# Kernel optimization log

Measured on AMD Instinct MI355X. Metric: run time of the kernel, lower is better.

The kernel has to match this reference:

```python
import jax, jax.numpy as jnp
import numpy as np

N = 100000
E = 1600000
D_IN = 128
HID = 128
LN_EPS = 1e-5
GIN_EPS = 0.0  # PyG GINConv default eps


def setup_inputs() -> dict:
    key = jax.random.key(0)
    ks = jax.random.split(key, 8)
    x = jax.random.normal(ks[0], (N, D_IN), dtype=jnp.float32)
    edge_index = jax.random.randint(ks[1], (2, E), 0, N, dtype=jnp.int64)
    s1 = 1.0 / np.sqrt(D_IN)
    s2 = 1.0 / np.sqrt(HID)
    W1 = jax.random.uniform(ks[2], (D_IN, HID), jnp.float32, -s1, s1)
    b1 = jnp.zeros((HID,), jnp.float32)
    W2 = jax.random.uniform(ks[3], (HID, HID), jnp.float32, -s2, s2)
    b2 = jnp.zeros((HID,), jnp.float32)
    gamma = jnp.ones((HID,), jnp.float32)
    beta = jnp.zeros((HID,), jnp.float32)
    Wres = jax.random.uniform(ks[4], (D_IN, HID), jnp.float32, -s1, s1)
    bres = jnp.zeros((HID,), jnp.float32)
    return {"x": x, "edge_index": edge_index, "W1": W1, "b1": b1,
            "W2": W2, "b2": b2, "gamma": gamma, "beta": beta,
            "Wres": Wres, "bres": bres}


def reference(x, edge_index, W1, b1, W2, b2, gamma, beta, Wres, bres):
    src, dst = edge_index[0], edge_index[1]
    # GIN sum aggregation: scatter-add source features onto targets. [N, D_IN]
    agg = jax.ops.segment_sum(x[src], dst, num_segments=N)
    h = (1.0 + GIN_EPS) * x + agg
    # GIN MLP: Linear -> ReLU -> Linear
    h = jax.nn.relu(h @ W1 + b1) @ W2 + b2
    # LayerNorm over hidden dim
    mu = jnp.mean(h, axis=-1, keepdims=True)
    var = jnp.mean(jnp.square(h - mu), axis=-1, keepdims=True)
    h = (h - mu) * jax.lax.rsqrt(var + LN_EPS) * gamma + beta
    # dropout p=0 is identity; residual linear path
    return h + (x @ Wres + bres)
```

## Files before the change

kernel.cpp:

```cpp
#include <hip/hip_runtime.h>

#define NN 100000
#define NE 1600000
#define D 128
#define RT 64
#define NB 196
#define CAP 9216
#define PADB 136
#define PB 12503
#define BUCKB 391

typedef unsigned short u16;
typedef __attribute__((ext_vector_type(8))) short bf16x8;
typedef __attribute__((ext_vector_type(4))) float f32x4;

__device__ __forceinline__ u16 f2bf(float f) {
  unsigned int u = __float_as_uint(f);
  u += 0x7fffu + ((u >> 16) & 1u);
  return (u16)(u >> 16);
}

__global__ __launch_bounds__(256) void prep_bucket_kernel(
    const float* __restrict__ x, const int* __restrict__ ei,
    const float* __restrict__ W1, const float* __restrict__ W2,
    const float* __restrict__ Wres,
    u16* __restrict__ xh, u16* __restrict__ wt,
    int* __restrict__ tail, unsigned* __restrict__ buf) {
  __shared__ int lhist[NB], lbase[NB];
  int b = blockIdx.x;
  int t = threadIdx.x;
  if (b < 12500) {
    int q = b * 256 + t;
    float4 v = ((const float4*)x)[q];
    uint2 pk;
    pk.x = (unsigned)f2bf(v.x) | ((unsigned)f2bf(v.y) << 16);
    pk.y = (unsigned)f2bf(v.z) | ((unsigned)f2bf(v.w) << 16);
    ((uint2*)xh)[q] = pk;
  } else if (b < PB) {
    const float* W = (b == 12500) ? Wres : (b == 12501) ? W1 : W2;
    u16* dst = wt + (size_t)(b - 12500) * 16384;
    for (int i = t; i < 16384; i += 256) {
      int n = i >> 7, k = i & 127;
      dst[i] = f2bf(W[k * 128 + n]);
    }
  } else {
    size_t e0 = (size_t)(b - PB) * 4096;
    int s[16], d[16];
    for (int j = t; j < NB; j += 256) lhist[j] = 0;
    __syncthreads();
#pragma unroll
    for (int k = 0; k < 16; ++k) {
      size_t e = e0 + t + (size_t)k * 256;
      if (e < NE) {
        d[k] = ei[NE + e];
        s[k] = ei[e];
        atomicAdd(&lhist[d[k] >> 9], 1);
      } else {
        d[k] = -1;
      }
    }
    __syncthreads();
    for (int j = t; j < NB; j += 256) {
      int c = lhist[j];
      lbase[j] = c ? atomicAdd(&tail[j], c) : 0;
      lhist[j] = 0;
    }
    __syncthreads();
#pragma unroll
    for (int k = 0; k < 16; ++k) {
      if (d[k] >= 0) {
        int bk = d[k] >> 9;
        int r = lbase[bk] + atomicAdd(&lhist[bk], 1);
        if (r < CAP)
          buf[(size_t)bk * CAP + r] = (unsigned)s[k] | ((unsigned)(d[k] & 511) << 17);
      }
    }
  }
}

__global__ __launch_bounds__(512) void build_csr(const unsigned* __restrict__ buf,
                                                 const int* __restrict__ tail,
                                                 int* __restrict__ cnt,
                                                 int* __restrict__ start,
                                                 int* __restrict__ csr) {
  __shared__ int lhist[512], lpre[512], lsum[64];
  int b = blockIdx.x, t = threadIdx.x;
  int nE = tail[b];
  if (nE > CAP) nE = CAP;
  size_t bBase = (size_t)b * CAP;
  lhist[t] = 0;
  __syncthreads();
  for (int i = t; i < nE; i += 512)
    atomicAdd(&lhist[buf[bBase + i] >> 17], 1);
  __syncthreads();
  if (t < 64) {
    int s = 0;
#pragma unroll
    for (int k = 0; k < 8; ++k) { int v = lhist[t * 8 + k]; lpre[t * 8 + k] = s; s += v; }
    lsum[t] = s;
  }
  __syncthreads();
  if (t == 0) {
    int s = 0;
    for (int k = 0; k < 64; ++k) { int v = lsum[k]; lsum[k] = s; s += v; }
  }
  __syncthreads();
  if (t < 64) {
    int o = lsum[t];
#pragma unroll
    for (int k = 0; k < 8; ++k) lpre[t * 8 + k] += o;
  }
  __syncthreads();
  int node = (b << 9) + t;
  if (node < NN) {
    cnt[node] = lhist[t];
    start[node] = (int)bBase + lpre[t];
  }
  lhist[t] = 0;
  __syncthreads();
  for (int i = t; i < nE; i += 512) {
    unsigned e = buf[bBase + i];
    int dl = e >> 17;
    int r = atomicAdd(&lhist[dl], 1);
    csr[bBase + lpre[dl] + r] = (int)(e & 0x1FFFFu);
  }
}

#define BFACC8(aL, aH, v)                                  \
  { aL.x += __uint_as_float((v).x << 16);                  \
    aL.y += __uint_as_float((v).x & 0xffff0000u);          \
    aL.z += __uint_as_float((v).y << 16);                  \
    aL.w += __uint_as_float((v).y & 0xffff0000u);          \
    aH.x += __uint_as_float((v).z << 16);                  \
    aH.y += __uint_as_float((v).z & 0xffff0000u);          \
    aH.z += __uint_as_float((v).w << 16);                  \
    aH.w += __uint_as_float((v).w & 0xffff0000u); }

__global__ __launch_bounds__(256, 6) void gather_kernel(const float* __restrict__ x,
                                                        const u16* __restrict__ xh,
                                                        const int* __restrict__ cnt,
                                                        const int* __restrict__ start,
                                                        const int* __restrict__ csr,
                                                        u16* __restrict__ h0h) {
  int g = blockIdx.x * 16 + (threadIdx.x >> 4);
  if (g >= NN) return;
  int lane = threadIdx.x & 15;
  int fo = lane * 8;
  int n = cnt[g];
  const int* sp = csr + start[g];

  float4 aL0 = make_float4(0.f, 0.f, 0.f, 0.f);
  float4 aH0 = aL0, aL1 = aL0, aH1 = aL0;

  int nfull = n & ~3;
  if (nfull > 0) {
    int s0 = sp[0], s1 = sp[1], s2 = sp[2], s3 = sp[3];
    uint4 v0 = *(const uint4*)&xh[(size_t)s0 * D + fo];
    uint4 v1 = *(const uint4*)&xh[(size_t)s1 * D + fo];
    uint4 v2 = *(const uint4*)&xh[(size_t)s2 * D + fo];
    uint4 v3 = *(const uint4*)&xh[(size_t)s3 * D + fo];
#pragma unroll 2
    for (int j = 4; j < nfull; j += 4) {
      int t0 = sp[j], t1 = sp[j + 1], t2 = sp[j + 2], t3 = sp[j + 3];
      uint4 w0 = *(const uint4*)&xh[(size_t)t0 * D + fo];
      uint4 w1 = *(const uint4*)&xh[(size_t)t1 * D + fo];
      uint4 w2 = *(const uint4*)&xh[(size_t)t2 * D + fo];
      uint4 w3 = *(const uint4*)&xh[(size_t)t3 * D + fo];
      BFACC8(aL0, aH0, v0); BFACC8(aL1, aH1, v1);
      BFACC8(aL0, aH0, v2); BFACC8(aL1, aH1, v3);
      v0 = w0; v1 = w1; v2 = w2; v3 = w3;
    }
    BFACC8(aL0, aH0, v0); BFACC8(aL1, aH1, v1);
    BFACC8(aL0, aH0, v2); BFACC8(aL1, aH1, v3);
  }
  for (int j = nfull; j < n; ++j) {
    uint4 v0 = *(const uint4*)&xh[(size_t)sp[j] * D + fo];
    BFACC8(aL0, aH0, v0);
  }

  const float* xp = &x[(size_t)g * D + fo];
  float4 x0 = *(const float4*)xp;
  float4 x1 = *(const float4*)(xp + 4);
  float h0 = x0.x + aL0.x + aL1.x;
  float h1 = x0.y + aL0.y + aL1.y;
  float h2 = x0.z + aL0.z + aL1.z;
  float h3 = x0.w + aL0.w + aL1.w;
  float h4 = x1.x + aH0.x + aH1.x;
  float h5 = x1.y + aH0.y + aH1.y;
  float h6 = x1.z + aH0.z + aH1.z;
  float h7 = x1.w + aH0.w + aH1.w;
  uint4 pk;
  pk.x = (unsigned)f2bf(h0) | ((unsigned)f2bf(h1) << 16);
  pk.y = (unsigned)f2bf(h2) | ((unsigned)f2bf(h3) << 16);
  pk.z = (unsigned)f2bf(h4) | ((unsigned)f2bf(h5) << 16);
  pk.w = (unsigned)f2bf(h6) | ((unsigned)f2bf(h7) << 16);
  *(uint4*)&h0h[(size_t)g * 256 + fo] = pk;
}

__global__ __launch_bounds__(256, 3) void fused_kernel(
    const u16* __restrict__ xh, const u16* __restrict__ h0h,
    const u16* __restrict__ wt,
    const float* __restrict__ b1, const float* __restrict__ b2,
    const float* __restrict__ gamma, const float* __restrict__ beta,
    const float* __restrict__ bres, float* __restrict__ out) {
  __shared__ u16 Ws[128 * PADB];
  __shared__ u16 Hs[RT * PADB];

  const int t = threadIdx.x;
  const int w = t >> 6;
  const int lane = t & 63;
  const int quad = lane >> 4;
  const int l16 = lane & 15;
  const int row0 = blockIdx.x * RT;

  auto stageW = [&](const u16* __restrict__ src) {
#pragma unroll
    for (int i = 0; i < 16; ++i) {
      int v = t + i * 256;
      int r = v >> 5;
      int c4 = (v & 31) << 2;
      *(uint2*)&Ws[r * PADB + c4] = *(const uint2*)&src[r * D + c4];
    }
  };

  f32x4 acc[8], accR[8];
  f32x4 zz = {0.f, 0.f, 0.f, 0.f};
#pragma unroll
  for (int i = 0; i < 8; ++i) { acc[i] = zz; accR[i] = zz; }

  auto gemmGA = [&](const u16* __restrict__ Ag, int astride, f32x4 (&dd)[8]) {
    bf16x8 af[4];
    int ar = row0 + w * 16 + l16;
    if (ar > NN - 1) ar = NN - 1;
#pragma unroll
    for (int s = 0; s < 4; ++s)
      af[s] = *(const bf16x8*)&Ag[(size_t)ar * astride + s * 32 + quad * 8];
#pragma unroll
    for (int nt = 0; nt < 8; ++nt) {
      const u16* wp = &Ws[(nt * 16 + l16) * PADB + quad * 8];
#pragma unroll
      for (int s = 0; s < 4; ++s) {
        bf16x8 bf = *(const bf16x8*)&wp[s * 32];
        dd[nt] = __builtin_amdgcn_mfma_f32_16x16x32_bf16(af[s], bf, dd[nt], 0, 0, 0);
      }
    }
  };
  auto gemmLA = [&](f32x4 (&dd)[8]) {
    bf16x8 af[4];
#pragma unroll
    for (int s = 0; s < 4; ++s)
      af[s] = *(const bf16x8*)&Hs[(w * 16 + l16) * PADB + s * 32 + quad * 8];
#pragma unroll
    for (int nt = 0; nt < 8; ++nt) {
      const u16* wp = &Ws[(nt * 16 + l16) * PADB + quad * 8];
#pragma unroll
      for (int s = 0; s < 4; ++s) {
        bf16x8 bf = *(const bf16x8*)&wp[s * 32];
        dd[nt] = __builtin_amdgcn_mfma_f32_16x16x32_bf16(af[s], bf, dd[nt], 0, 0, 0);
      }
    }
  };

  stageW(wt);
  __syncthreads();
  gemmGA(xh, D, accR);
  __syncthreads();
  stageW(wt + 16384);
  __syncthreads();
  gemmGA(h0h, 256, acc);
  __syncthreads();

#pragma unroll
  for (int nt = 0; nt < 8; ++nt) {
    int col = nt * 16 + l16;
    float bb = b1[col];
#pragma unroll
    for (int r = 0; r < 4; ++r) {
      float hv = acc[nt][r] + bb;
      hv = hv > 0.f ? hv : 0.f;
      Hs[(w * 16 + quad * 4 + r) * PADB + col] = f2bf(hv);
      acc[nt][r] = 0.f;
    }
  }
  stageW(wt + 32768);
  __syncthreads();
  gemmLA(acc);

  float b2v[8], gv[8], bev[8], brv[8];
#pragma unroll
  for (int nt = 0; nt < 8; ++nt) {
    int col = nt * 16 + l16;
    b2v[nt] = b2[col];
    gv[nt] = gamma[col];
    bev[nt] = beta[col];
    brv[nt] = bres[col];
  }
#pragma unroll
  for (int r = 0; r < 4; ++r) {
    float s = 0.f, s2 = 0.f;
#pragma unroll
    for (int nt = 0; nt < 8; ++nt) {
      float h = acc[nt][r] + b2v[nt];
      s += h;
      s2 += h * h;
    }
    for (int m = 1; m <= 8; m <<= 1) {
      s += __shfl_xor(s, m);
      s2 += __shfl_xor(s2, m);
    }
    float mu = s * 0.0078125f;
    float var = s2 * 0.0078125f - mu * mu;
    float rs = rsqrtf(var + 1e-5f);
    int row = row0 + w * 16 + quad * 4 + r;
    if (row < NN) {
#pragma unroll
      for (int nt = 0; nt < 8; ++nt) {
        float h = acc[nt][r] + b2v[nt];
        out[(size_t)row * D + nt * 16 + l16] =
            (h - mu) * rs * gv[nt] + bev[nt] + accR[nt][r] + brv[nt];
      }
    }
  }
}

extern "C" void kernel_launch(void* const* d_in, const int* in_sizes, int n_in,
                              void* d_out, int out_size, void* d_ws, size_t ws_size,
                              hipStream_t stream) {
  const float* x     = (const float*)d_in[0];
  const int*   ei    = (const int*)d_in[1];
  const float* W1    = (const float*)d_in[2];
  const float* b1    = (const float*)d_in[3];
  const float* W2    = (const float*)d_in[4];
  const float* b2    = (const float*)d_in[5];
  const float* gamma = (const float*)d_in[6];
  const float* beta  = (const float*)d_in[7];
  const float* Wres  = (const float*)d_in[8];
  const float* bres  = (const float*)d_in[9];
  float* out = (float*)d_out;

  int*      tail  = (int*)d_ws;
  unsigned* buf   = (unsigned*)(tail + 256);
  int*      cnt   = (int*)(buf + (size_t)NB * CAP);
  int*      start = cnt + NN;
  int*      csr   = start + NN;
  u16*      xh    = (u16*)(csr + (size_t)NB * CAP);
  u16*      wt    = xh + (size_t)NN * D;

  u16* h0h = (u16*)out;

  hipMemsetAsync(tail, 0, 256 * sizeof(int), stream);
  prep_bucket_kernel<<<PB + BUCKB, 256, 0, stream>>>(x, ei, W1, W2, Wres,
                                                     xh, wt, tail, buf);
  build_csr<<<NB, 512, 0, stream>>>(buf, tail, cnt, start, csr);
  gather_kernel<<<(NN + 15) / 16, 256, 0, stream>>>(x, xh, cnt, start, csr, h0h);
  fused_kernel<<<(NN + RT - 1) / RT, 256, 0, stream>>>(
      xh, h0h, wt, b1, b2, gamma, beta, bres, out);
}
```

Before: 256.0 us.

## Merge prep, bucketing and CSR build into one cooperative kernel with grid syncs

Replaces the memset plus the prep/bucket kernel and the build_csr kernel with a single cooperative kernel of 196 blocks of 512 threads. Grid-wide syncs separate the edge histogram, bucket scatter and CSR construction phases, and the tail counters are zeroed inside the kernel and padded apart. This removes two launches and the memset gap, but runs the bf16 conversion of x and the edge work on only 196 blocks instead of about 12,900. That may lower parallelism and latency hiding, and the grid syncs add their own cost.

Result: slower. 419.8 us (+64.0%).

```diff
diff --git a/kernel.cpp b/kernel.cpp
--- a/kernel.cpp
+++ b/kernel.cpp
@@ -1,4 +1,7 @@
 #include <hip/hip_runtime.h>
+#include <hip/hip_cooperative_groups.h>
+
+namespace cg = cooperative_groups;
 
 #define NN 100000
 #define NE 1600000
@@ -7,8 +10,8 @@
 #define NB 196
 #define CAP 9216
 #define PADB 136
-#define PB 12503
-#define BUCKB 391
+#define TS 16
+#define EPB 8164
 
 typedef unsigned short u16;
 typedef __attribute__((ext_vector_type(8))) short bf16x8;
@@ -20,72 +23,73 @@
   return (u16)(u >> 16);
 }
 
-__global__ __launch_bounds__(256) void prep_bucket_kernel(
+__global__ __launch_bounds__(512) void preproc_kernel(
     const float* __restrict__ x, const int* __restrict__ ei,
     const float* __restrict__ W1, const float* __restrict__ W2,
     const float* __restrict__ Wres,
     u16* __restrict__ xh, u16* __restrict__ wt,
-    int* __restrict__ tail, unsigned* __restrict__ buf) {
-  __shared__ int lhist[NB], lbase[NB];
-  int b = blockIdx.x;
-  int t = threadIdx.x;
-  if (b < 12500) {
-    int q = b * 256 + t;
+    int* __restrict__ tail, unsigned* __restrict__ buf,
+    int* __restrict__ cnt, int* __restrict__ start, int* __restrict__ csr) {
+  __shared__ int lhist[512], lpre[512], lsum[64], lbase[NB];
+  cg::grid_group grid = cg::this_grid();
+  const int b = blockIdx.x;
+  const int t = threadIdx.x;
+  const int tid = b * 512 + t;
+
+  if (t == 0) tail[b * TS] = 0;
+
+  for (int j = t; j < NB; j += 512) lhist[j] = 0;
+  __syncthreads();
+  int s_[16], d_[16];
+  size_t e0 = (size_t)b * EPB;
+  size_t e1 = e0 + EPB; if (e1 > NE) e1 = NE;
+#pragma unroll
+  for (int k = 0; k < 16; ++k) {
+    size_t e = e0 + t + (size_t)k * 512;
+    if (e < e1) {
+      d_[k] = ei[NE + e];
+      s_[k] = ei[e];
+      atomicAdd(&lhist[d_[k] >> 9], 1);
+    } else {
+      d_[k] = -1;
+    }
+  }
+
+  for (int q = tid; q < 3200000; q += NB * 512) {
     float4 v = ((const float4*)x)[q];
     uint2 pk;
     pk.x = (unsigned)f2bf(v.x) | ((unsigned)f2bf(v.y) << 16);
     pk.y = (unsigned)f2bf(v.z) | ((unsigned)f2bf(v.w) << 16);
     ((uint2*)xh)[q] = pk;
-  } else if (b < PB) {
-    const float* W = (b == 12500) ? Wres : (b == 12501) ? W1 : W2;
-    u16* dst = wt + (size_t)(b - 12500) * 16384;
-    for (int i = t; i < 16384; i += 256) {
-      int n = i >> 7, k = i & 127;
-      dst[i] = f2bf(W[k * 128 + n]);
-    }
-  } else {
-    size_t e0 = (size_t)(b - PB) * 4096;
-    int s[16], d[16];
-    for (int j = t; j < NB; j += 256) lhist[j] = 0;
-    __syncthreads();
-#pragma unroll
-    for (int k = 0; k < 16; ++k) {
-      size_t e = e0 + t + (size_t)k * 256;
-      if (e < NE) {
-        d[k] = ei[NE + e];
-        s[k] = ei[e];
-        atomicAdd(&lhist[d[k] >> 9], 1);
-      } else {
-        d[k] = -1;
-      }
-    }
-    __syncthreads();
-    for (int j = t; j < NB; j += 256) {
-      int c = lhist[j];
-      lbase[j] = c ? atomicAdd(&tail[j], c) : 0;
-      lhist[j] = 0;
-    }
-    __syncthreads();
-#pragma unroll
-    for (int k = 0; k < 16; ++k) {
-      if (d[k] >= 0) {
-        int bk = d[k] >> 9;
-        int r = lbase[bk] + atomicAdd(&lhist[bk], 1);
-        if (r < CAP)
-          buf[(size_t)bk * CAP + r] = (unsigned)s[k] | ((unsigned)(d[k] & 511) << 17);
-      }
-    }
-  }
-}
-
-__global__ __launch_bounds__(512) void build_csr(const unsigned* __restrict__ buf,
-                                                 const int* __restrict__ tail,
-                                                 int* __restrict__ cnt,
-                                                 int* __restrict__ start,
-                                                 int* __restrict__ csr) {
-  __shared__ int lhist[512], lpre[512], lsum[64];
-  int b = blockIdx.x, t = threadIdx.x;
-  int nE = tail[b];
+  }
+  if (tid < 49152) {
+    int wsel = tid >> 14, i = tid & 16383;
+    const float* W = (wsel == 0) ? Wres : (wsel == 1) ? W1 : W2;
+    int n = i >> 7, k = i & 127;
+    wt[wsel * 16384 + i] = f2bf(W[k * 128 + n]);
+  }
+
+  __threadfence();
+  grid.sync();
+
+  if (t < NB) lbase[t] = lhist[t] ? atomicAdd(&tail[t * TS], lhist[t]) : 0;
+  __syncthreads();
+  if (t < NB) lhist[t] = 0;
+  __syncthreads();
+#pragma unroll
+  for (int k = 0; k < 16; ++k) {
+    if (d_[k] >= 0) {
+      int bk = d_[k] >> 9;
+      int r = lbase[bk] + atomicAdd(&lhist[bk], 1);
+      if (r < CAP)
+        buf[(size_t)bk * CAP + r] = (unsigned)s_[k] | ((unsigned)(d_[k] & 511) << 17);
+    }
+  }
+
+  __threadfence();
+  grid.sync();
+
+  int nE = tail[b * TS];
   if (nE > CAP) nE = CAP;
   size_t bBase = (size_t)b * CAP;
   lhist[t] = 0;
@@ -339,7 +343,7 @@
   float* out = (float*)d_out;
 
   int*      tail  = (int*)d_ws;
-  unsigned* buf   = (unsigned*)(tail + 256);
+  unsigned* buf   = (unsigned*)(tail + NB * TS);
   int*      cnt   = (int*)(buf + (size_t)NB * CAP);
   int*      start = cnt + NN;
   int*      csr   = start + NN;
@@ -348,10 +352,11 @@
 
   u16* h0h = (u16*)out;
 
-  hipMemsetAsync(tail, 0, 256 * sizeof(int), stream);
-  prep_bucket_kernel<<<PB + BUCKB, 256, 0, stream>>>(x, ei, W1, W2, Wres,
-                                                     xh, wt, tail, buf);
-  build_csr<<<NB, 512, 0, stream>>>(buf, tail, cnt, start, csr);
+  void* args[] = {(void*)&x, (void*)&ei, (void*)&W1, (void*)&W2, (void*)&Wres,
+                  (void*)&xh, (void*)&wt, (void*)&tail, (void*)&buf,
+                  (void*)&cnt, (void*)&start, (void*)&csr};
+  hipLaunchCooperativeKernel((const void*)preproc_kernel, dim3(NB), dim3(512),
+                             args, 0, stream);
   gather_kernel<<<(NN + 15) / 16, 256, 0, stream>>>(x, xh, cnt, start, csr, h0h);
   fused_kernel<<<(NN + RT - 1) / RT, 256, 0, stream>>>(
       xh, h0h, wt, b1, b2, gamma, beta, bres, out);
```

## Split prep kernel into grid-stride convert and separate bucket kernel, pad tail counters

Applied to the files above, without the earlier changes.

Splits the combined convert/bucketing kernel into two launches: a grid-stride bf16 conversion kernel with 2048 blocks plus three weight-transpose blocks, and a standalone edge-bucketing kernel. The per-bucket global tail counters are padded 16 ints apart so the global atomics from different buckets land on separate cache lines. The aim is to cut block-scheduling overhead from the 12.5k one-shot conversion blocks and reduce atomic contention on the counters. The cost is an extra kernel launch, and the bucketing work can no longer overlap with conversion inside a single grid.

New measurement: 257.9 us. About the same (+0.8%).

```diff
diff --git a/kernel.cpp b/kernel.cpp
--- a/kernel.cpp
+++ b/kernel.cpp
@@ -7,8 +7,9 @@
 #define NB 196
 #define CAP 9216
 #define PADB 136
-#define PB 12503
-#define BUCKB 391
+#define TS 16
+#define CVB 2048
+#define BKB 391
 
 typedef unsigned short u16;
 typedef __attribute__((ext_vector_type(8))) short bf16x8;
@@ -20,60 +21,65 @@
   return (u16)(u >> 16);
 }
 
-__global__ __launch_bounds__(256) void prep_bucket_kernel(
-    const float* __restrict__ x, const int* __restrict__ ei,
+__global__ __launch_bounds__(256) void prep_convert(
+    const float* __restrict__ x,
     const float* __restrict__ W1, const float* __restrict__ W2,
     const float* __restrict__ Wres,
-    u16* __restrict__ xh, u16* __restrict__ wt,
-    int* __restrict__ tail, unsigned* __restrict__ buf) {
-  __shared__ int lhist[NB], lbase[NB];
+    u16* __restrict__ xh, u16* __restrict__ wt) {
   int b = blockIdx.x;
   int t = threadIdx.x;
-  if (b < 12500) {
-    int q = b * 256 + t;
-    float4 v = ((const float4*)x)[q];
-    uint2 pk;
-    pk.x = (unsigned)f2bf(v.x) | ((unsigned)f2bf(v.y) << 16);
-    pk.y = (unsigned)f2bf(v.z) | ((unsigned)f2bf(v.w) << 16);
-    ((uint2*)xh)[q] = pk;
-  } else if (b < PB) {
-    const float* W = (b == 12500) ? Wres : (b == 12501) ? W1 : W2;
-    u16* dst = wt + (size_t)(b - 12500) * 16384;
+  if (b < CVB) {
+    for (int q = b * 256 + t; q < 3200000; q += CVB * 256) {
+      float4 v = ((const float4*)x)[q];
+      uint2 pk;
+      pk.x = (unsigned)f2bf(v.x) | ((unsigned)f2bf(v.y) << 16);
+      pk.y = (unsigned)f2bf(v.z) | ((unsigned)f2bf(v.w) << 16);
+      ((uint2*)xh)[q] = pk;
+    }
+  } else {
+    const float* W = (b == CVB) ? Wres : (b == CVB + 1) ? W1 : W2;
+    u16* dst = wt + (size_t)(b - CVB) * 16384;
     for (int i = t; i < 16384; i += 256) {
       int n = i >> 7, k = i & 127;
       dst[i] = f2bf(W[k * 128 + n]);
     }
-  } else {
-    size_t e0 = (size_t)(b - PB) * 4096;
-    int s[16], d[16];
-    for (int j = t; j < NB; j += 256) lhist[j] = 0;
-    __syncthreads();
-#pragma unroll
-    for (int k = 0; k < 16; ++k) {
-      size_t e = e0 + t + (size_t)k * 256;
-      if (e < NE) {
-        d[k] = ei[NE + e];
-        s[k] = ei[e];
-        atomicAdd(&lhist[d[k] >> 9], 1);
-      } else {
-        d[k] = -1;
-      }
-    }
-    __syncthreads();
-    for (int j = t; j < NB; j += 256) {
-      int c = lhist[j];
-      lbase[j] = c ? atomicAdd(&tail[j], c) : 0;
-      lhist[j] = 0;
-    }
-    __syncthreads();
-#pragma unroll
-    for (int k = 0; k < 16; ++k) {
-      if (d[k] >= 0) {
-        int bk = d[k] >> 9;
-        int r = lbase[bk] + atomicAdd(&lhist[bk], 1);
-        if (r < CAP)
-          buf[(size_t)bk * CAP + r] = (unsigned)s[k] | ((unsigned)(d[k] & 511) << 17);
-      }
+  }
+}
+
+__global__ __launch_bounds__(256) void bucket_kernel(const int* __restrict__ ei,
+                                                     int* __restrict__ tail,
+                                                     unsigned* __restrict__ buf) {
+  __shared__ int lhist[NB], lbase[NB];
+  int t = threadIdx.x;
+  size_t e0 = (size_t)blockIdx.x * 4096;
+  int s_[16], d_[16];
+  for (int j = t; j < NB; j += 256) lhist[j] = 0;
+  __syncthreads();
+#pragma unroll
+  for (int k = 0; k < 16; ++k) {
+    size_t e = e0 + t + (size_t)k * 256;
+    if (e < NE) {
+      d_[k] = ei[NE + e];
+      s_[k] = ei[e];
+      atomicAdd(&lhist[d_[k] >> 9], 1);
+    } else {
+      d_[k] = -1;
+    }
+  }
+  __syncthreads();
+  for (int j = t; j < NB; j += 256) {
+    int c = lhist[j];
+    lbase[j] = c ? atomicAdd(&tail[j * TS], c) : 0;
+    lhist[j] = 0;
+  }
+  __syncthreads();
+#pragma unroll
+  for (int k = 0; k < 16; ++k) {
+    if (d_[k] >= 0) {
+      int bk = d_[k] >> 9;
+      int r = lbase[bk] + atomicAdd(&lhist[bk], 1);
+      if (r < CAP)
+        buf[(size_t)bk * CAP + r] = (unsigned)s_[k] | ((unsigned)(d_[k] & 511) << 17);
     }
   }
 }
@@ -85,7 +91,7 @@
                                                  int* __restrict__ csr) {
   __shared__ int lhist[512], lpre[512], lsum[64];
   int b = blockIdx.x, t = threadIdx.x;
-  int nE = tail[b];
+  int nE = tail[b * TS];
   if (nE > CAP) nE = CAP;
   size_t bBase = (size_t)b * CAP;
   lhist[t] = 0;
@@ -339,7 +345,7 @@
   float* out = (float*)d_out;
 
   int*      tail  = (int*)d_ws;
-  unsigned* buf   = (unsigned*)(tail + 256);
+  unsigned* buf   = (unsigned*)(tail + NB * TS);
   int*      cnt   = (int*)(buf + (size_t)NB * CAP);
   int*      start = cnt + NN;
   int*      csr   = start + NN;
@@ -348,9 +354,9 @@
 
   u16* h0h = (u16*)out;
 
-  hipMemsetAsync(tail, 0, 256 * sizeof(int), stream);
-  prep_bucket_kernel<<<PB + BUCKB, 256, 0, stream>>>(x, ei, W1, W2, Wres,
-                                                     xh, wt, tail, buf);
+  hipMemsetAsync(tail, 0, NB * TS * sizeof(int), stream);
+  prep_convert<<<CVB + 3, 256, 0, stream>>>(x, W1, W2, Wres, xh, wt);
+  bucket_kernel<<<BKB, 256, 0, stream>>>(ei, tail, buf);
   build_csr<<<NB, 512, 0, stream>>>(buf, tail, cnt, start, csr);
   gather_kernel<<<(NN + 15) / 16, 256, 0, stream>>>(x, xh, cnt, start, csr, h0h);
   fused_kernel<<<(NN + RT - 1) / RT, 256, 0, stream>>>(
```
